# Optimization experiments

Hardware: AMD Instinct MI355X
Metric: run time of the kernel (lower is better)

## Reference

```python
import jax, jax.numpy as jnp
import numpy as np

B, N, K = 4, 2048, 30
H = 128   # num_hidden == num_V_dim
E = 128   # num_E_dim
SCALE = 30.0
EPS = 1e-5


def _ln(x, g, b):
    m = jnp.mean(x, axis=-1, keepdims=True)
    v = jnp.mean(jnp.square(x - m), axis=-1, keepdims=True)
    return (x - m) * jax.lax.rsqrt(v + EPS) * g + b


def _gather_nodes(h_V, E_idx):
    # h_V: [B,N,D], E_idx: [B,N,K] -> [B,N,K,D]
    b, n, k = E_idx.shape
    flat = E_idx.reshape(b, n * k)
    g = jnp.take_along_axis(h_V, flat[:, :, None], axis=1)
    return g.reshape(b, n, k, h_V.shape[-1])


def _gelu(x):
    return jax.nn.gelu(x, approximate=False)  # torch GELU default (erf)


def _lin(x, w, b):
    return jnp.einsum('...i,oi->...o', x, w) + b


def setup_inputs() -> dict:
    key = jax.random.key(0)
    ks = jax.random.split(key, 24)
    s = 0.05
    inp = {
        'h_V': jax.random.normal(ks[0], (B, N, H), jnp.float32),
        'h_E': jax.random.normal(ks[1], (B, N, K, E), jnp.float32),
        'E_idx': jax.random.randint(ks[2], (B, N, K), 0, N, jnp.int32),
        'mask_V': jnp.ones((B, N), jnp.float32),
        'mask_attend': jnp.ones((B, N, K), jnp.float32),
        # node-update MLP W1,W2,W3
        'W1_w': jax.random.normal(ks[3], (H, E + 2 * H), jnp.float32) * s,
        'W1_b': jnp.zeros((H,), jnp.float32),
        'W2_w': jax.random.normal(ks[4], (H, H), jnp.float32) * s,
        'W2_b': jnp.zeros((H,), jnp.float32),
        'W3_w': jax.random.normal(ks[5], (H, H), jnp.float32) * s,
        'W3_b': jnp.zeros((H,), jnp.float32),
        # edge-update MLP W11,W12,W13
        'W11_w': jax.random.normal(ks[6], (H, E + 2 * H), jnp.float32) * s,
        'W11_b': jnp.zeros((H,), jnp.float32),
        'W12_w': jax.random.normal(ks[7], (H, H), jnp.float32) * s,
        'W12_b': jnp.zeros((H,), jnp.float32),
        'W13_w': jax.random.normal(ks[8], (E, H), jnp.float32) * s,
        'W13_b': jnp.zeros((E,), jnp.float32),
        # dense FFN
        'Win_w': jax.random.normal(ks[9], (4 * H, H), jnp.float32) * s,
        'Win_b': jnp.zeros((4 * H,), jnp.float32),
        'Wout_w': jax.random.normal(ks[10], (H, 4 * H), jnp.float32) * s,
        'Wout_b': jnp.zeros((H,), jnp.float32),
        # layer norms
        'g1': jnp.ones((H,), jnp.float32), 'b1': jnp.zeros((H,), jnp.float32),
        'g2': jnp.ones((H,), jnp.float32), 'b2': jnp.zeros((H,), jnp.float32),
        'g3': jnp.ones((E,), jnp.float32), 'b3': jnp.zeros((E,), jnp.float32),
    }
    return inp


def reference(h_V, h_E, E_idx, mask_V, mask_attend,
              W1_w, W1_b, W2_w, W2_b, W3_w, W3_b,
              W11_w, W11_b, W12_w, W12_b, W13_w, W13_b,
              Win_w, Win_b, Wout_w, Wout_b,
              g1, b1, g2, b2, g3, b3):
    # --- node update ---
    nb = _gather_nodes(h_V, E_idx)                               # [B,N,K,H]
    hV_exp = jnp.broadcast_to(h_V[:, :, None, :], nb.shape)
    h_EV = jnp.concatenate([hV_exp, h_E, nb], axis=-1)           # [B,N,K,E+2H]
    m = _lin(_gelu(_lin(_gelu(_lin(h_EV, W1_w, W1_b)), W2_w, W2_b)), W3_w, W3_b)
    m = mask_attend[..., None] * m
    dh = jnp.sum(m, axis=-2) / SCALE
    h_V = _ln(h_V + dh, g1, b1)
    dh = _lin(_gelu(_lin(h_V, Win_w, Win_b)), Wout_w, Wout_b)
    h_V = _ln(h_V + dh, g2, b2)
    h_V = mask_V[..., None] * h_V
    # --- edge update ---
    nb = _gather_nodes(h_V, E_idx)
    hV_exp = jnp.broadcast_to(h_V[:, :, None, :], nb.shape)
    h_EV = jnp.concatenate([hV_exp, h_E, nb], axis=-1)
    m = _lin(_gelu(_lin(_gelu(_lin(h_EV, W11_w, W11_b)), W12_w, W12_b)), W13_w, W13_b)
    h_E = _ln(h_E + m, g3, b3)
    return h_V, h_E
```

## Files before the change

### kernel.cpp

```cpp
#include <hip/hip_runtime.h>
#include <math.h>

#define Kn    30
#define Hn    128
#define NB    2048
#define YS    136

#define OFF_W1    0
#define OFF_W2    49152
#define OFF_W3    65536
#define OFF_W11   81920
#define OFF_W12   131072
#define OFF_W13   147456
#define OFF_WIN   163840
#define OFF_WOUT  229376
#define W_TOTAL   294912
#define WS_HMID   0
#define WS_SS     1048576
#define WS_SN     2097152

typedef __attribute__((ext_vector_type(8)))  short bh8;
typedef __attribute__((ext_vector_type(4)))  short bh4;
typedef __attribute__((ext_vector_type(16))) float fx16;

__device__ __forceinline__ unsigned short f2bf(float f) {
    unsigned int u = __float_as_uint(f);
    u += 0x7fffu + ((u >> 16) & 1u);
    return (unsigned short)(u >> 16);
}
__device__ __forceinline__ float bf2f(unsigned short h) {
    return __uint_as_float(((unsigned int)h) << 16);
}
__device__ __forceinline__ float gelu_f(float x) {
    float u = 0.7978845608028654f * x * (1.0f + 0.044715f * x * x);
    return x / (1.0f + __expf(-2.0f * u));
}
__device__ __forceinline__ fx16 mfma_bf16(bh8 a, bh8 b, fx16 c) {
    return __builtin_amdgcn_mfma_f32_32x32x16_bf16(a, b, c, 0, 0, 0);
}
__device__ __forceinline__ void st_bf4(unsigned short* dst, float4 v) {
    bh4 t;
    t.x = (short)f2bf(v.x); t.y = (short)f2bf(v.y);
    t.z = (short)f2bf(v.z); t.w = (short)f2bf(v.w);
    *(bh4*)dst = t;
}

template<int KS>
__device__ __forceinline__ void gemm_pair(const unsigned short* __restrict__ aBase,
                                          const unsigned short* __restrict__ b0,
                                          const unsigned short* __restrict__ b1,
                                          fx16& acc0, fx16& acc1) {
    #pragma unroll
    for (int ks = 0; ks < KS; ks++) {
        bh8 a = *(const bh8*)(aBase + ks * 16);
        acc0 = mfma_bf16(a, *(const bh8*)(b0 + ks * 16), acc0);
        acc1 = mfma_bf16(a, *(const bh8*)(b1 + ks * 16), acc1);
    }
}

__device__ __forceinline__ void epi_gelu_sp(const fx16& ac, int col, int rowBase,
                                            float bias, const float* __restrict__ sSelf,
                                            const float* pre,
                                            unsigned short* __restrict__ dst, int lane) {
    int ro = rowBase + 4 * (lane >> 5);
    #pragma unroll
    for (int r = 0; r < 16; r++) {
        int row = ro + (r & 3) + 8 * (r >> 2);
        float st = sSelf[((row >= Kn) ? 128 : 0) + col];
        dst[row * YS + col] = f2bf(gelu_f(ac[r] + bias + st + pre[r]));
    }
}
__device__ __forceinline__ void epi_gelu(const fx16& ac, int col, int rowBase,
                                         float bias, unsigned short* __restrict__ dst,
                                         int lane) {
    int ro = rowBase + 4 * (lane >> 5);
    #pragma unroll
    for (int r = 0; r < 16; r++) {
        int row = ro + (r & 3) + 8 * (r >> 2);
        dst[row * YS + col] = f2bf(gelu_f(ac[r] + bias));
    }
}
__device__ __forceinline__ void epi_plain(const fx16& ac, int col, int rowBase,
                                          float bias, unsigned short* __restrict__ dst,
                                          int lane) {
    int ro = rowBase + 4 * (lane >> 5);
    #pragma unroll
    for (int r = 0; r < 16; r++) {
        int row = ro + (r & 3) + 8 * (r >> 2);
        dst[row * YS + col] = f2bf(ac[r] + bias);
    }
}

__global__ __launch_bounds__(256) void prep_weights(
    const float* __restrict__ W1, const float* __restrict__ W2,
    const float* __restrict__ W3, const float* __restrict__ W11,
    const float* __restrict__ W12, const float* __restrict__ W13,
    const float* __restrict__ Win, const float* __restrict__ Wout,
    unsigned short* __restrict__ wsbf) {
    int i = blockIdx.x * 256 + threadIdx.x;
    if (i >= W_TOTAL) return;
    float v;
    if      (i < OFF_W2)   v = W1[i - OFF_W1];
    else if (i < OFF_W3)   v = W2[i - OFF_W2];
    else if (i < OFF_W11)  v = W3[i - OFF_W3];
    else if (i < OFF_W12)  v = W11[i - OFF_W11];
    else if (i < OFF_W13)  v = W12[i - OFF_W12];
    else if (i < OFF_WIN)  v = W13[i - OFF_W13];
    else if (i < OFF_WOUT) v = Win[i - OFF_WIN];
    else                   v = Wout[i - OFF_WOUT];
    wsbf[i] = f2bf(v);
}

__global__ __launch_bounds__(256) void self_gemm(
    const float* __restrict__ hv, const unsigned short* __restrict__ wsbf,
    float* __restrict__ s1s, float* __restrict__ s1n) {
    __shared__ __align__(16) unsigned short sA[32 * YS];
    const int tid = threadIdx.x;
    const int p0 = blockIdx.x * 32;
    const unsigned short* W1bf = wsbf + OFF_W1;
    for (int i = tid; i < 1024; i += 256) {
        int r = i >> 5, c4 = (i & 31) << 2;
        float4 v = *(const float4*)(hv + (size_t)(p0 + r) * Hn + c4);
        st_bf4(sA + r * YS + c4, v);
    }
    __syncthreads();
    const int wid = tid >> 6, lane = tid & 63;
    const int lane31 = lane & 31, lk = (lane >> 5) << 3;
    fx16 accS = {}, accN = {};
    const unsigned short* a   = sA + lane31 * YS + lk;
    const unsigned short* bwS = W1bf + (size_t)(32 * wid + lane31) * 384 + lk;
    const unsigned short* bwN = bwS + 256;
    #pragma unroll
    for (int ks = 0; ks < 8; ks++) {
        bh8 av = *(const bh8*)(a + ks * 16);
        accS = mfma_bf16(av, *(const bh8*)(bwS + ks * 16), accS);
        accN = mfma_bf16(av, *(const bh8*)(bwN + ks * 16), accN);
    }
    int col = 32 * wid + lane31;
    #pragma unroll
    for (int r = 0; r < 16; r++) {
        int row = (r & 3) + 8 * (r >> 2) + 4 * (lane >> 5);
        s1s[(size_t)(p0 + row) * Hn + col] = accS[r];
        s1n[(size_t)(p0 + row) * Hn + col] = accN[r];
    }
}

__global__ __launch_bounds__(256, 4) void node_update_mfma(
    const float* __restrict__ h_V, const float* __restrict__ h_E,
    const int* __restrict__ E_idx, const float* __restrict__ mask_attend,
    const unsigned short* __restrict__ wsbf,
    const float* __restrict__ s1s, const float* __restrict__ s1n,
    const float* __restrict__ W1_b, const float* __restrict__ W2_b,
    const float* __restrict__ W3_b,
    const float* __restrict__ g1v, const float* __restrict__ b1v,
    float* __restrict__ hmid) {
    __shared__ __align__(16) unsigned short sX[64 * YS];
    __shared__ __align__(16) unsigned short sY[64 * YS];
    __shared__ float sS1[256];
    __shared__ float sMask[64];
    __shared__ int   sIdx[64];
    __shared__ float sStats[4];

    const int tid = threadIdx.x;
    const int p0 = blockIdx.x * 2;
    const int bB = p0 >> 11;
    const unsigned short* W1bf = wsbf + OFF_W1;
    const unsigned short* W2bf = wsbf + OFF_W2;
    const unsigned short* W3bf = wsbf + OFF_W3;

    for (int i = tid; i < 1920; i += 256) {
        int r = i >> 5, c4 = (i & 31) << 2;
        float4 v = *(const float4*)(h_E + ((size_t)(p0 * Kn + r)) * Hn + c4);
        st_bf4(sX + r * YS + c4, v);
    }
    for (int i = tid; i < 272; i += 256)
        ((unsigned int*)(sX + 60 * YS))[i] = 0;
    if (tid < 64) {
        int g = tid >> 5, c4 = (tid & 31) << 2;
        *(float4*)(sS1 + g * 128 + c4) = *(const float4*)(s1s + (size_t)(p0 + g) * Hn + c4);
    }
    if (tid < 60) sMask[tid] = mask_attend[p0 * Kn + tid];
    if (tid < 64) sIdx[tid] = (tid < 60) ? E_idx[p0 * Kn + tid] : 0;
    __syncthreads();

    const int wid = tid >> 6, lane = tid & 63;
    const int mt = wid & 1, np = wid >> 1;
    const int lane31 = lane & 31, lk = (lane >> 5) << 3;
    const int rowBase = 32 * mt;
    const fx16 zv = {};
    const int c0 = 64 * np + lane31, c1 = c0 + 32;

    float pre0[16], pre1[16];
    #pragma unroll
    for (int r = 0; r < 16; r++) {
        int row = rowBase + 4 * (lane >> 5) + (r & 3) + 8 * (r >> 2);
        const float* sp = s1n + (size_t)(bB * NB + sIdx[row]) * Hn;
        pre0[r] = sp[c0];
        pre1[r] = sp[c1];
    }

    fx16 acc0 = zv, acc1 = zv;
    gemm_pair<8>(sX + (rowBase + lane31) * YS + lk,
                 W1bf + (64 * np + lane31) * 384 + 128 + lk,
                 W1bf + (64 * np + 32 + lane31) * 384 + 128 + lk, acc0, acc1);
    epi_gelu_sp(acc0, c0, rowBase, W1_b[c0], sS1, pre0, sY, lane);
    epi_gelu_sp(acc1, c1, rowBase, W1_b[c1], sS1, pre1, sY, lane);
    __syncthreads();

    acc0 = zv; acc1 = zv;
    gemm_pair<8>(sY + (rowBase + lane31) * YS + lk,
                 W2bf + (64 * np + lane31) * 128 + lk,
                 W2bf + (64 * np + 32 + lane31) * 128 + lk, acc0, acc1);
    __syncthreads();
    epi_gelu(acc0, c0, rowBase, W2_b[c0], sY, lane);
    epi_gelu(acc1, c1, rowBase, W2_b[c1], sY, lane);
    __syncthreads();

    acc0 = zv; acc1 = zv;
    gemm_pair<8>(sY + (rowBase + lane31) * YS + lk,
                 W3bf + (64 * np + lane31) * 128 + lk,
                 W3bf + (64 * np + 32 + lane31) * 128 + lk, acc0, acc1);
    float* fbuf = (float*)sX;
    #pragma unroll
    for (int t = 0; t < 2; t++) {
        const fx16& ac = t ? acc1 : acc0;
        int col = t ? c1 : c0;
        float bias = W3_b[col];
        float sA0 = 0.f, sA1 = 0.f;
        #pragma unroll
        for (int r = 0; r < 16; r++) {
            int row = rowBase + (r & 3) + 8 * (r >> 2) + 4 * (lane >> 5);
            if (row < 60) {
                float v = (ac[r] + bias) * sMask[row];
                if (row < Kn) sA0 += v; else sA1 += v;
            }
        }
        sA0 += __shfl_down(sA0, 32);
        sA1 += __shfl_down(sA1, 32);
        if (lane < 32) { fbuf[mt * 256 + col] = sA0; fbuf[mt * 256 + 128 + col] = sA1; }
    }
    __syncthreads();

    float* xbuf = fbuf + 512;
    {
        int g = tid >> 7, c = tid & 127;
        float x = h_V[(size_t)(p0 + g) * Hn + c] +
                  (fbuf[g * 128 + c] + fbuf[256 + g * 128 + c]) * (1.0f / 30.0f);
        xbuf[g * 128 + c] = x;
    }
    __syncthreads();
    if (wid < 2) {
        float x0 = xbuf[wid * 128 + lane], x1 = xbuf[wid * 128 + 64 + lane];
        float s = x0 + x1, q = x0 * x0 + x1 * x1;
        #pragma unroll
        for (int off = 32; off; off >>= 1) { s += __shfl_down(s, off); q += __shfl_down(q, off); }
        if (lane == 0) {
            float mean = s * 0.0078125f;
            sStats[wid * 2] = mean;
            sStats[wid * 2 + 1] = rsqrtf(q * 0.0078125f - mean * mean + 1e-5f);
        }
    }
    __syncthreads();
    {
        int g = tid >> 7, c = tid & 127;
        float hv = (xbuf[g * 128 + c] - sStats[g * 2]) * sStats[g * 2 + 1] * g1v[c] + b1v[c];
        hmid[(size_t)(p0 + g) * Hn + c] = hv;
    }
}

__global__ __launch_bounds__(256) void ffn_fused(
    const float* __restrict__ hmid, const float* __restrict__ mask_V,
    const unsigned short* __restrict__ wsbf,
    const float* __restrict__ Win_b, const float* __restrict__ Wout_b,
    const float* __restrict__ g2v, const float* __restrict__ b2v,
    float* __restrict__ hV_out, float* __restrict__ s11s, float* __restrict__ s11n) {
    __shared__ __align__(16) unsigned short sA[32 * YS];
    __shared__ __align__(16) unsigned short sH[32 * YS];
    __shared__ __align__(16) float sO[32 * 132];
    __shared__ __align__(16) unsigned short sV[32 * YS];

    const int tid = threadIdx.x;
    const int p0 = blockIdx.x * 32;
    const unsigned short* Winbf  = wsbf + OFF_WIN;
    const unsigned short* Woutbf = wsbf + OFF_WOUT;
    const unsigned short* W11bf  = wsbf + OFF_W11;

    for (int i = tid; i < 1024; i += 256) {
        int r = i >> 5, c4 = (i & 31) << 2;
        float4 v = *(const float4*)(hmid + (size_t)(p0 + r) * Hn + c4);
        st_bf4(sA + r * YS + c4, v);
    }
    __syncthreads();

    const int wid = tid >> 6, lane = tid & 63;
    const int lane31 = lane & 31, lk = (lane >> 5) << 3;
    const fx16 zv = {};
    fx16 accO = zv;

    for (int c = 0; c < 4; c++) {
        int hcol = 128 * c + 32 * wid + lane31;
        fx16 t = zv;
        {
            const unsigned short* a  = sA + lane31 * YS + lk;
            const unsigned short* bw = Winbf + (size_t)hcol * 128 + lk;
            #pragma unroll
            for (int ks = 0; ks < 8; ks++)
                t = mfma_bf16(*(const bh8*)(a + ks * 16), *(const bh8*)(bw + ks * 16), t);
        }
        float bias = Win_b[hcol];
        int colL = 32 * wid + lane31;
        #pragma unroll
        for (int r = 0; r < 16; r++) {
            int row = (r & 3) + 8 * (r >> 2) + 4 * (lane >> 5);
            sH[row * YS + colL] = f2bf(gelu_f(t[r] + bias));
        }
        __syncthreads();
        {
            const unsigned short* a  = sH + lane31 * YS + lk;
            const unsigned short* bw = Woutbf + (size_t)(32 * wid + lane31) * 512 + 128 * c + lk;
            #pragma unroll
            for (int ks = 0; ks < 8; ks++)
                accO = mfma_bf16(*(const bh8*)(a + ks * 16), *(const bh8*)(bw + ks * 16), accO);
        }
        __syncthreads();
    }
    {
        int col = 32 * wid + lane31;
        float bias = Wout_b[col];
        #pragma unroll
        for (int r = 0; r < 16; r++) {
            int row = (r & 3) + 8 * (r >> 2) + 4 * (lane >> 5);
            sO[row * 132 + col] = accO[r] + bias;
        }
    }
    __syncthreads();
    for (int r = wid; r < 32; r += 4) {
        float x0 = sO[r * 132 + lane]      + hmid[(size_t)(p0 + r) * Hn + lane];
        float x1 = sO[r * 132 + 64 + lane] + hmid[(size_t)(p0 + r) * Hn + 64 + lane];
        float s = x0 + x1, q = x0 * x0 + x1 * x1;
        #pragma unroll
        for (int off = 32; off; off >>= 1) { s += __shfl_down(s, off); q += __shfl_down(q, off); }
        s = __shfl(s, 0); q = __shfl(q, 0);
        float mean = s * 0.0078125f;
        float rstd = rsqrtf(q * 0.0078125f - mean * mean + 1e-5f);
        float mv = mask_V[p0 + r];
        float y0 = ((x0 - mean) * rstd * g2v[lane]      + b2v[lane])      * mv;
        float y1 = ((x1 - mean) * rstd * g2v[lane + 64] + b2v[lane + 64]) * mv;
        hV_out[(size_t)(p0 + r) * Hn + lane]      = y0;
        hV_out[(size_t)(p0 + r) * Hn + 64 + lane] = y1;
        sV[r * YS + lane]      = f2bf(y0);
        sV[r * YS + 64 + lane] = f2bf(y1);
    }
    __syncthreads();
    {
        int col = 32 * wid + lane31;
        fx16 accS = zv, accN = zv;
        const unsigned short* a   = sV + lane31 * YS + lk;
        const unsigned short* bwS = W11bf + (size_t)col * 384 + lk;
        const unsigned short* bwN = W11bf + (size_t)col * 384 + 256 + lk;
        #pragma unroll
        for (int ks = 0; ks < 8; ks++) {
            bh8 av = *(const bh8*)(a + ks * 16);
            accS = mfma_bf16(av, *(const bh8*)(bwS + ks * 16), accS);
            accN = mfma_bf16(av, *(const bh8*)(bwN + ks * 16), accN);
        }
        #pragma unroll
        for (int r = 0; r < 16; r++) {
            int row = (r & 3) + 8 * (r >> 2) + 4 * (lane >> 5);
            s11s[(size_t)(p0 + row) * Hn + col] = accS[r];
            s11n[(size_t)(p0 + row) * Hn + col] = accN[r];
        }
    }
}

__global__ __launch_bounds__(256, 4) void edge_update_mfma(
    const float* __restrict__ h_E, const int* __restrict__ E_idx,
    const unsigned short* __restrict__ wsbf,
    const float* __restrict__ s11s, const float* __restrict__ s11n,
    const float* __restrict__ W11_b, const float* __restrict__ W12_b,
    const float* __restrict__ W13_b,
    const float* __restrict__ g3v, const float* __restrict__ b3v,
    float* __restrict__ hE_out) {
    __shared__ __align__(16) unsigned short sX[64 * YS];
    __shared__ __align__(16) unsigned short sY[64 * YS];
    __shared__ float sS11[256];
    __shared__ int   sIdx[64];

    const int tid = threadIdx.x;
    const int p0 = blockIdx.x * 2;
    const int bB = p0 >> 11;
    const unsigned short* W11bf = wsbf + OFF_W11;
    const unsigned short* W12bf = wsbf + OFF_W12;
    const unsigned short* W13bf = wsbf + OFF_W13;

    for (int i = tid; i < 1920; i += 256) {
        int r = i >> 5, c4 = (i & 31) << 2;
        float4 v = *(const float4*)(h_E + ((size_t)(p0 * Kn + r)) * Hn + c4);
        st_bf4(sX + r * YS + c4, v);
    }
    for (int i = tid; i < 272; i += 256)
        ((unsigned int*)(sX + 60 * YS))[i] = 0;
    if (tid < 64) {
        int g = tid >> 5, c4 = (tid & 31) << 2;
        *(float4*)(sS11 + g * 128 + c4) = *(const float4*)(s11s + (size_t)(p0 + g) * Hn + c4);
    }
    if (tid < 64) sIdx[tid] = (tid < 60) ? E_idx[p0 * Kn + tid] : 0;
    __syncthreads();

    const int wid = tid >> 6, lane = tid & 63;
    const int mt = wid & 1, np = wid >> 1;
    const int lane31 = lane & 31, lk = (lane >> 5) << 3;
    const int rowBase = 32 * mt;
    const fx16 zv = {};
    const int c0 = 64 * np + lane31, c1 = c0 + 32;

    float pre0[16], pre1[16];
    #pragma unroll
    for (int r = 0; r < 16; r++) {
        int row = rowBase + 4 * (lane >> 5) + (r & 3) + 8 * (r >> 2);
        const float* sp = s11n + (size_t)(bB * NB + sIdx[row]) * Hn;
        pre0[r] = sp[c0];
        pre1[r] = sp[c1];
    }

    fx16 acc0 = zv, acc1 = zv;
    gemm_pair<8>(sX + (rowBase + lane31) * YS + lk,
                 W11bf + (64 * np + lane31) * 384 + 128 + lk,
                 W11bf + (64 * np + 32 + lane31) * 384 + 128 + lk, acc0, acc1);
    epi_gelu_sp(acc0, c0, rowBase, W11_b[c0], sS11, pre0, sY, lane);
    epi_gelu_sp(acc1, c1, rowBase, W11_b[c1], sS11, pre1, sY, lane);
    __syncthreads();

    acc0 = zv; acc1 = zv;
    gemm_pair<8>(sY + (rowBase + lane31) * YS + lk,
                 W12bf + (64 * np + lane31) * 128 + lk,
                 W12bf + (64 * np + 32 + lane31) * 128 + lk, acc0, acc1);
    __syncthreads();
    epi_gelu(acc0, c0, rowBase, W12_b[c0], sY, lane);
    epi_gelu(acc1, c1, rowBase, W12_b[c1], sY, lane);
    __syncthreads();

    acc0 = zv; acc1 = zv;
    gemm_pair<8>(sY + (rowBase + lane31) * YS + lk,
                 W13bf + (64 * np + lane31) * 128 + lk,
                 W13bf + (64 * np + 32 + lane31) * 128 + lk, acc0, acc1);
    __syncthreads();
    epi_plain(acc0, c0, rowBase, W13_b[c0], sY, lane);
    epi_plain(acc1, c1, rowBase, W13_b[c1], sY, lane);
    __syncthreads();

    for (int r = wid; r < 60; r += 4) {
        float x0 = bf2f(sX[r * YS + lane])      + bf2f(sY[r * YS + lane]);
        float x1 = bf2f(sX[r * YS + 64 + lane]) + bf2f(sY[r * YS + 64 + lane]);
        float s = x0 + x1, q = x0 * x0 + x1 * x1;
        #pragma unroll
        for (int off = 32; off; off >>= 1) { s += __shfl_down(s, off); q += __shfl_down(q, off); }
        s = __shfl(s, 0); q = __shfl(q, 0);
        float mean = s * 0.0078125f;
        float rstd = rsqrtf(q * 0.0078125f - mean * mean + 1e-5f);
        float* op = hE_out + ((size_t)(p0 * Kn + r)) * 128;
        op[lane]      = (x0 - mean) * rstd * g3v[lane]      + b3v[lane];
        op[lane + 64] = (x1 - mean) * rstd * g3v[lane + 64] + b3v[lane + 64];
    }
}

extern "C" void kernel_launch(void* const* d_in, const int* in_sizes, int n_in,
                              void* d_out, int out_size, void* d_ws, size_t ws_size,
                              hipStream_t stream) {
    const float* h_V         = (const float*)d_in[0];
    const float* h_E         = (const float*)d_in[1];
    const int*   E_idx       = (const int*)  d_in[2];
    const float* mask_V      = (const float*)d_in[3];
    const float* mask_attend = (const float*)d_in[4];
    const float* W1_w  = (const float*)d_in[5];
    const float* W1_b  = (const float*)d_in[6];
    const float* W2_w  = (const float*)d_in[7];
    const float* W2_b  = (const float*)d_in[8];
    const float* W3_w  = (const float*)d_in[9];
    const float* W3_b  = (const float*)d_in[10];
    const float* W11_w = (const float*)d_in[11];
    const float* W11_b = (const float*)d_in[12];
    const float* W12_w = (const float*)d_in[13];
    const float* W12_b = (const float*)d_in[14];
    const float* W13_w = (const float*)d_in[15];
    const float* W13_b = (const float*)d_in[16];
    const float* Win_w  = (const float*)d_in[17];
    const float* Win_b  = (const float*)d_in[18];
    const float* Wout_w = (const float*)d_in[19];
    const float* Wout_b = (const float*)d_in[20];
    const float* g1 = (const float*)d_in[21];
    const float* b1 = (const float*)d_in[22];
    const float* g2 = (const float*)d_in[23];
    const float* b2 = (const float*)d_in[24];
    const float* g3 = (const float*)d_in[25];
    const float* b3 = (const float*)d_in[26];

    float* out    = (float*)d_out;
    float* hV_out = out;
    float* hE_out = out + (size_t)4 * 2048 * 128;
    unsigned short* wsbf = (unsigned short*)d_ws;
    float* wsf  = (float*)(wsbf + W_TOTAL);
    float* hmid = wsf + WS_HMID;
    float* sS   = wsf + WS_SS;
    float* sN   = wsf + WS_SN;

    prep_weights<<<(W_TOTAL + 255) / 256, 256, 0, stream>>>(
        W1_w, W2_w, W3_w, W11_w, W12_w, W13_w, Win_w, Wout_w, wsbf);

    self_gemm<<<256, 256, 0, stream>>>(h_V, wsbf, sS, sN);

    node_update_mfma<<<4096, 256, 0, stream>>>(
        h_V, h_E, E_idx, mask_attend, wsbf, sS, sN,
        W1_b, W2_b, W3_b, g1, b1, hmid);

    ffn_fused<<<256, 256, 0, stream>>>(
        hmid, mask_V, wsbf, Win_b, Wout_b, g2, b2, hV_out, sS, sN);

    edge_update_mfma<<<4096, 256, 0, stream>>>(
        h_E, E_idx, wsbf, sS, sN,
        W11_b, W12_b, W13_b, g3, b3, hE_out);
}
```

Before: 526.5 us.

## Apply W3 after the neighbor sum to shrink the per-edge GEMM chain

Because W3 is linear, the masked sum over K neighbors is taken on the GELU(W2) activations first. W3 then runs once per node inside the FFN kernel, and its bias is scaled by the mean mask. This removes one 128x128 GEMM per edge and two block syncs from the per-edge node kernel. The LayerNorm1 work moves into the FFN kernel. The summed activations are stored as bf16, which adds a small precision cost.

```diff
diff --git a/kernel.cpp b/kernel.cpp
--- a/kernel.cpp
+++ b/kernel.cpp
@@ -15,7 +15,7 @@
 #define OFF_WIN   163840
 #define OFF_WOUT  229376
 #define W_TOTAL   294912
-#define WS_HMID   0
+#define WS_ZM     524288
 #define WS_SS     1048576
 #define WS_SN     2097152
 
@@ -145,28 +145,24 @@
     }
 }
 
-__global__ __launch_bounds__(256, 4) void node_update_mfma(
-    const float* __restrict__ h_V, const float* __restrict__ h_E,
-    const int* __restrict__ E_idx, const float* __restrict__ mask_attend,
+__global__ __launch_bounds__(256, 4) void node_msg_mfma(
+    const float* __restrict__ h_E, const int* __restrict__ E_idx,
+    const float* __restrict__ mask_attend,
     const unsigned short* __restrict__ wsbf,
     const float* __restrict__ s1s, const float* __restrict__ s1n,
     const float* __restrict__ W1_b, const float* __restrict__ W2_b,
-    const float* __restrict__ W3_b,
-    const float* __restrict__ g1v, const float* __restrict__ b1v,
-    float* __restrict__ hmid) {
+    unsigned short* __restrict__ zbf, float* __restrict__ zm) {
     __shared__ __align__(16) unsigned short sX[64 * YS];
     __shared__ __align__(16) unsigned short sY[64 * YS];
     __shared__ float sS1[256];
     __shared__ float sMask[64];
     __shared__ int   sIdx[64];
-    __shared__ float sStats[4];
 
     const int tid = threadIdx.x;
     const int p0 = blockIdx.x * 2;
     const int bB = p0 >> 11;
     const unsigned short* W1bf = wsbf + OFF_W1;
     const unsigned short* W2bf = wsbf + OFF_W2;
-    const unsigned short* W3bf = wsbf + OFF_W3;
 
     for (int i = tid; i < 1920; i += 256) {
         int r = i >> 5, c4 = (i & 31) << 2;
@@ -211,27 +207,18 @@
     gemm_pair<8>(sY + (rowBase + lane31) * YS + lk,
                  W2bf + (64 * np + lane31) * 128 + lk,
                  W2bf + (64 * np + 32 + lane31) * 128 + lk, acc0, acc1);
-    __syncthreads();
-    epi_gelu(acc0, c0, rowBase, W2_b[c0], sY, lane);
-    epi_gelu(acc1, c1, rowBase, W2_b[c1], sY, lane);
-    __syncthreads();
-
-    acc0 = zv; acc1 = zv;
-    gemm_pair<8>(sY + (rowBase + lane31) * YS + lk,
-                 W3bf + (64 * np + lane31) * 128 + lk,
-                 W3bf + (64 * np + 32 + lane31) * 128 + lk, acc0, acc1);
     float* fbuf = (float*)sX;
     #pragma unroll
     for (int t = 0; t < 2; t++) {
         const fx16& ac = t ? acc1 : acc0;
         int col = t ? c1 : c0;
-        float bias = W3_b[col];
+        float bias = W2_b[col];
         float sA0 = 0.f, sA1 = 0.f;
         #pragma unroll
         for (int r = 0; r < 16; r++) {
             int row = rowBase + (r & 3) + 8 * (r >> 2) + 4 * (lane >> 5);
             if (row < 60) {
-                float v = (ac[r] + bias) * sMask[row];
+                float v = gelu_f(ac[r] + bias) * sMask[row];
                 if (row < Kn) sA0 += v; else sA1 += v;
             }
         }
@@ -241,62 +228,89 @@
     }
     __syncthreads();
 
-    float* xbuf = fbuf + 512;
     {
         int g = tid >> 7, c = tid & 127;
-        float x = h_V[(size_t)(p0 + g) * Hn + c] +
-                  (fbuf[g * 128 + c] + fbuf[256 + g * 128 + c]) * (1.0f / 30.0f);
-        xbuf[g * 128 + c] = x;
-    }
-    __syncthreads();
-    if (wid < 2) {
-        float x0 = xbuf[wid * 128 + lane], x1 = xbuf[wid * 128 + 64 + lane];
-        float s = x0 + x1, q = x0 * x0 + x1 * x1;
-        #pragma unroll
-        for (int off = 32; off; off >>= 1) { s += __shfl_down(s, off); q += __shfl_down(q, off); }
-        if (lane == 0) {
-            float mean = s * 0.0078125f;
-            sStats[wid * 2] = mean;
-            sStats[wid * 2 + 1] = rsqrtf(q * 0.0078125f - mean * mean + 1e-5f);
-        }
-    }
-    __syncthreads();
-    {
-        int g = tid >> 7, c = tid & 127;
-        float hv = (xbuf[g * 128 + c] - sStats[g * 2]) * sStats[g * 2 + 1] * g1v[c] + b1v[c];
-        hmid[(size_t)(p0 + g) * Hn + c] = hv;
-    }
-}
-
-__global__ __launch_bounds__(256) void ffn_fused(
-    const float* __restrict__ hmid, const float* __restrict__ mask_V,
+        float zval = (fbuf[g * 128 + c] + fbuf[256 + g * 128 + c]) * (1.0f / 30.0f);
+        zbf[(size_t)(p0 + g) * Hn + c] = f2bf(zval);
+    }
+    if (tid < 2) {
+        float s = 0.f;
+        #pragma unroll
+        for (int k = 0; k < 30; k++) s += sMask[tid * 30 + k];
+        zm[p0 + tid] = s * (1.0f / 30.0f);
+    }
+}
+
+__global__ __launch_bounds__(256) void node_fin_ffn(
+    const unsigned short* __restrict__ zbf, const float* __restrict__ zm,
+    const float* __restrict__ h_V, const float* __restrict__ mask_V,
     const unsigned short* __restrict__ wsbf,
-    const float* __restrict__ Win_b, const float* __restrict__ Wout_b,
+    const float* __restrict__ W3_b, const float* __restrict__ Win_b,
+    const float* __restrict__ Wout_b,
+    const float* __restrict__ g1v, const float* __restrict__ b1v,
     const float* __restrict__ g2v, const float* __restrict__ b2v,
     float* __restrict__ hV_out, float* __restrict__ s11s, float* __restrict__ s11n) {
     __shared__ __align__(16) unsigned short sA[32 * YS];
     __shared__ __align__(16) unsigned short sH[32 * YS];
     __shared__ __align__(16) float sO[32 * 132];
+    __shared__ __align__(16) float sM[32 * 132];
     __shared__ __align__(16) unsigned short sV[32 * YS];
+    __shared__ float sZm[32];
 
     const int tid = threadIdx.x;
     const int p0 = blockIdx.x * 32;
+    const unsigned short* W3bf   = wsbf + OFF_W3;
     const unsigned short* Winbf  = wsbf + OFF_WIN;
     const unsigned short* Woutbf = wsbf + OFF_WOUT;
     const unsigned short* W11bf  = wsbf + OFF_W11;
 
-    for (int i = tid; i < 1024; i += 256) {
-        int r = i >> 5, c4 = (i & 31) << 2;
-        float4 v = *(const float4*)(hmid + (size_t)(p0 + r) * Hn + c4);
-        st_bf4(sA + r * YS + c4, v);
-    }
+    for (int i = tid; i < 512; i += 256) {
+        int r = i >> 4, c8 = (i & 15) << 3;
+        *(bh8*)(sA + r * YS + c8) = *(const bh8*)(zbf + (size_t)(p0 + r) * Hn + c8);
+    }
+    if (tid < 32) sZm[tid] = zm[p0 + tid];
     __syncthreads();
 
     const int wid = tid >> 6, lane = tid & 63;
     const int lane31 = lane & 31, lk = (lane >> 5) << 3;
     const fx16 zv = {};
+
+    {
+        fx16 acc = zv;
+        const unsigned short* a  = sA + lane31 * YS + lk;
+        const unsigned short* bw = W3bf + (size_t)(32 * wid + lane31) * 128 + lk;
+        #pragma unroll
+        for (int ks = 0; ks < 8; ks++)
+            acc = mfma_bf16(*(const bh8*)(a + ks * 16), *(const bh8*)(bw + ks * 16), acc);
+        int col = 32 * wid + lane31;
+        float bias = W3_b[col];
+        #pragma unroll
+        for (int r = 0; r < 16; r++) {
+            int row = (r & 3) + 8 * (r >> 2) + 4 * (lane >> 5);
+            sO[row * 132 + col] = acc[r] + sZm[row] * bias;
+        }
+    }
+    __syncthreads();
+
+    for (int r = wid; r < 32; r += 4) {
+        float x0 = sO[r * 132 + lane]      + h_V[(size_t)(p0 + r) * Hn + lane];
+        float x1 = sO[r * 132 + 64 + lane] + h_V[(size_t)(p0 + r) * Hn + 64 + lane];
+        float s = x0 + x1, q = x0 * x0 + x1 * x1;
+        #pragma unroll
+        for (int off = 32; off; off >>= 1) { s += __shfl_down(s, off); q += __shfl_down(q, off); }
+        s = __shfl(s, 0); q = __shfl(q, 0);
+        float mean = s * 0.0078125f;
+        float rstd = rsqrtf(q * 0.0078125f - mean * mean + 1e-5f);
+        float m0 = (x0 - mean) * rstd * g1v[lane]      + b1v[lane];
+        float m1 = (x1 - mean) * rstd * g1v[lane + 64] + b1v[lane + 64];
+        sM[r * 132 + lane]      = m0;
+        sM[r * 132 + 64 + lane] = m1;
+        sA[r * YS + lane]      = f2bf(m0);
+        sA[r * YS + 64 + lane] = f2bf(m1);
+    }
+    __syncthreads();
+
     fx16 accO = zv;
-
     for (int c = 0; c < 4; c++) {
         int hcol = 128 * c + 32 * wid + lane31;
         fx16 t = zv;
@@ -334,9 +348,10 @@
         }
     }
     __syncthreads();
+
     for (int r = wid; r < 32; r += 4) {
-        float x0 = sO[r * 132 + lane]      + hmid[(size_t)(p0 + r) * Hn + lane];
-        float x1 = sO[r * 132 + 64 + lane] + hmid[(size_t)(p0 + r) * Hn + 64 + lane];
+        float x0 = sO[r * 132 + lane]      + sM[r * 132 + lane];
+        float x1 = sO[r * 132 + 64 + lane] + sM[r * 132 + 64 + lane];
         float s = x0 + x1, q = x0 * x0 + x1 * x1;
         #pragma unroll
         for (int off = 32; off; off >>= 1) { s += __shfl_down(s, off); q += __shfl_down(q, off); }
@@ -352,6 +367,7 @@
         sV[r * YS + 64 + lane] = f2bf(y1);
     }
     __syncthreads();
+
     {
         int col = 32 * wid + lane31;
         fx16 accS = zv, accN = zv;
@@ -499,22 +515,23 @@
     float* hV_out = out;
     float* hE_out = out + (size_t)4 * 2048 * 128;
     unsigned short* wsbf = (unsigned short*)d_ws;
-    float* wsf  = (float*)(wsbf + W_TOTAL);
-    float* hmid = wsf + WS_HMID;
-    float* sS   = wsf + WS_SS;
-    float* sN   = wsf + WS_SN;
+    float* wsf = (float*)(wsbf + W_TOTAL);
+    unsigned short* zbf = (unsigned short*)wsf;
+    float* zm = wsf + WS_ZM;
+    float* sS = wsf + WS_SS;
+    float* sN = wsf + WS_SN;
 
     prep_weights<<<(W_TOTAL + 255) / 256, 256, 0, stream>>>(
         W1_w, W2_w, W3_w, W11_w, W12_w, W13_w, Win_w, Wout_w, wsbf);
 
     self_gemm<<<256, 256, 0, stream>>>(h_V, wsbf, sS, sN);
 
-    node_update_mfma<<<4096, 256, 0, stream>>>(
-        h_V, h_E, E_idx, mask_attend, wsbf, sS, sN,
-        W1_b, W2_b, W3_b, g1, b1, hmid);
-
-    ffn_fused<<<256, 256, 0, stream>>>(
-        hmid, mask_V, wsbf, Win_b, Wout_b, g2, b2, hV_out, sS, sN);
+    node_msg_mfma<<<4096, 256, 0, stream>>>(
+        h_E, E_idx, mask_attend, wsbf, sS, sN, W1_b, W2_b, zbf, zm);
+
+    node_fin_ffn<<<256, 256, 0, stream>>>(
+        zbf, zm, h_V, mask_V, wsbf, W3_b, Win_b, Wout_b,
+        g1, b1, g2, b2, hV_out, sS, sN);
 
     edge_update_mfma<<<4096, 256, 0, stream>>>(
         h_E, E_idx, wsbf, sS, sN,
```

Result: faster. 503.5 us (-4.4%).
